# Kernel tuning notes

Hardware: AMD Instinct MI355X
Metric: run time of the kernel (lower is better)

## Reference

```python
import jax, jax.numpy as jnp
import numpy as np

EPS = 1e-5
N, K, C = 32768, 27, 128


def setup_inputs() -> dict:
    key = jax.random.key(0)
    k1, k2, k3, k4 = jax.random.split(key, 4)
    feats = jax.random.normal(k1, (N, C), dtype=jnp.float32)
    # Precomputed kernel-offset neighbor map (MinkowskiEngine kernel map),
    # one input index per (point, kernel offset).
    neighbors = jax.random.randint(k2, (N, K), 0, N, dtype=jnp.int32)
    scale = 1.0 / np.sqrt(K * C)  # fan-in init like sparse conv
    W1 = jax.random.normal(k3, (K, C, C), dtype=jnp.float32) * scale
    W2 = jax.random.normal(k4, (K, C, C), dtype=jnp.float32) * scale
    g1 = jnp.ones((C,), jnp.float32)
    b1 = jnp.zeros((C,), jnp.float32)
    g2 = jnp.ones((C,), jnp.float32)
    b2 = jnp.zeros((C,), jnp.float32)
    return {"feats": feats, "neighbors": neighbors, "W1": W1, "g1": g1,
            "b1": b1, "W2": W2, "g2": g2, "b2": b2}


def _sparse_conv(f, nbr, W):
    # gather-GEMM-scatter: gather neighbor features per kernel offset,
    # contract with that offset's weight, sum over offsets.
    gathered = f[nbr]                      # [N, K, C]
    return jnp.einsum('nkc,kcd->nd', gathered, W)  # [N, C]


def _batch_norm(x, gamma, beta):
    mu = jnp.mean(x, axis=0)
    var = jnp.mean(jnp.square(x - mu), axis=0)
    return (x - mu) * jax.lax.rsqrt(var + EPS) * gamma + beta


def reference(feats, neighbors, W1, g1, b1, W2, g2, b2):
    out = _sparse_conv(feats, neighbors, W1)
    out = jax.nn.relu(_batch_norm(out, g1, b1))
    out = _sparse_conv(out, neighbors, W2)
    out = _batch_norm(out, g2, b2)
    return jax.nn.relu(out + feats)
```

## Files before the change

### kernel.cpp

```cpp
#include <hip/hip_runtime.h>
#include <stdint.h>

#define NPTS 32768
#define KOFF 27
#define CH   128
#define NC   (NPTS*CH)
#define TILE_M 64
#define NITER (KOFF*2)

typedef __attribute__((ext_vector_type(8))) short short8;
typedef __attribute__((ext_vector_type(4))) float f32x4;
typedef unsigned short u16;

__device__ __forceinline__ float bf2f(u16 u) {
    union { uint32_t i; float f; } v; v.i = ((uint32_t)u) << 16; return v.f;
}
__device__ __forceinline__ u16 f2bf(float f) {
    union { float f; uint32_t i; } v; v.f = f;
    return (u16)((v.i + 0x7FFF + ((v.i >> 16) & 1)) >> 16);
}

#define GLDS16(gp, lp) __builtin_amdgcn_global_load_lds( \
    (__attribute__((address_space(1))) void*)(gp),           \
    (__attribute__((address_space(3))) void*)(lp), 16, 0, 0)

__global__ __launch_bounds__(256)
void prep_kernel(const float* __restrict__ W1, const float* __restrict__ W2,
                 u16* __restrict__ W1t, u16* __restrict__ W2t,
                 const float* __restrict__ feats, u16* __restrict__ xbuf,
                 float* __restrict__ stat)
{
    __shared__ u16 t[128*129];
    const int b = blockIdx.x, tid = threadIdx.x;
    if (b < 2*KOFF) {
        if (b == 0) for (int i = tid; i < 512; i += 256) stat[i] = 0.0f;
        const float* src = (b < KOFF) ? W1 + (size_t)b*CH*CH : W2 + (size_t)(b-KOFF)*CH*CH;
        u16* dst         = (b < KOFF) ? W1t + (size_t)b*CH*CH : W2t + (size_t)(b-KOFF)*CH*CH;
        for (int e = tid; e < CH*CH; e += 256) {
            int c = e >> 7, d = e & 127;
            t[d*129 + c] = f2bf(src[e]);
        }
        __syncthreads();
        for (int e = tid; e < CH*CH; e += 256) {
            int d = e >> 7, c = e & 127;
            dst[e] = t[d*129 + c];
        }
    } else {
        size_t e = ((size_t)(b - 2*KOFF) * 256 + tid) * 8;
        float4 a = *(const float4*)(feats + e);
        float4 c = *(const float4*)(feats + e + 4);
        ushort4 lo, hi;
        lo.x = f2bf(a.x); lo.y = f2bf(a.y); lo.z = f2bf(a.z); lo.w = f2bf(a.w);
        hi.x = f2bf(c.x); hi.y = f2bf(c.y); hi.z = f2bf(c.z); hi.w = f2bf(c.w);
        *(ushort4*)(xbuf + e) = lo;
        *(ushort4*)(xbuf + e + 4) = hi;
    }
}

__global__ __launch_bounds__(256)
void ResidualBlock_77498389889548_kernel(const u16* __restrict__ xb,
                                         const int* __restrict__ nbr,
                                         const u16* __restrict__ Wt,
                                         u16* __restrict__ y,
                                         float* __restrict__ gsum,
                                         float* __restrict__ gsq)
{
    __shared__ __align__(16) u16 A_lds[2][TILE_M*64];
    __shared__ __align__(16) u16 B_lds[2][CH*64];
    __shared__ int idx_lds[KOFF*TILE_M];
    __shared__ float ls[CH], lq[CH];

    const int tid = threadIdx.x;
    const int n0  = blockIdx.x * TILE_M;

    if (tid < CH) { ls[tid] = 0.0f; lq[tid] = 0.0f; }
    for (int e = tid; e < KOFF*TILE_M; e += 256) {
        int kk = e >> 6, r = e & 63;
        int nb = nbr[(size_t)(n0 + r)*KOFF + kk];
        idx_lds[e] = ((unsigned)nb < (unsigned)NPTS) ? nb : 0;
    }
    __syncthreads();

    const int wave = tid >> 6;
    const int lane = tid & 63;
    const int wrow = (wave >> 1) * 32;
    const int wcol = (wave & 1) * 64;
    const int lm   = lane & 15;
    const int quad = lane >> 4;
    const int l8r  = lane >> 3;
    const int swz  = ((lane & 7) ^ l8r) << 3;

    f32x4 acc[2][4];
    #pragma unroll
    for (int i = 0; i < 2; ++i)
        #pragma unroll
        for (int j = 0; j < 4; ++j)
            #pragma unroll
            for (int r = 0; r < 4; ++r) acc[i][j][r] = 0.0f;

    int aoff[2][2], boff[2][4];
    #pragma unroll
    for (int kc = 0; kc < 2; ++kc) {
        int g = kc*4 + quad;
        #pragma unroll
        for (int i = 0; i < 2; ++i) {
            int row = wrow + i*16 + lm;
            aoff[kc][i] = row*128 + ((g ^ (row & 7)) << 4);
        }
        #pragma unroll
        for (int j = 0; j < 4; ++j) {
            int d = wcol + j*16 + lm;
            boff[kc][j] = d*128 + ((g ^ (d & 7)) << 4);
        }
    }

    auto stage = [&](int it, int b) {
        const int kk = it >> 1;
        const int h  = it & 1;
        #pragma unroll
        for (int j = 0; j < 2; ++j) {
            int row8 = wave*16 + j*8;
            int nb = idx_lds[kk*64 + row8 + l8r];
            GLDS16(xb + (size_t)nb*CH + h*64 + swz, &A_lds[b][row8*64]);
        }
        const u16* wb = Wt + (size_t)kk*CH*CH + h*64 + swz;
        #pragma unroll
        for (int j = 0; j < 4; ++j) {
            int row8 = wave*32 + j*8;
            GLDS16(wb + (size_t)(row8 + l8r)*CH, &B_lds[b][row8*64]);
        }
    };

    stage(0, 0);
    __syncthreads();

    for (int it = 0; it < NITER; ++it) {
        const int cur = it & 1;
        if (it + 1 < NITER) stage(it + 1, cur ^ 1);

        const char* Ab = (const char*)A_lds[cur];
        const char* Bb = (const char*)B_lds[cur];
        #pragma unroll
        for (int kc = 0; kc < 2; ++kc) {
            short8 a[2], b[4];
            #pragma unroll
            for (int i = 0; i < 2; ++i) a[i] = *(const short8*)(Ab + aoff[kc][i]);
            #pragma unroll
            for (int j = 0; j < 4; ++j) b[j] = *(const short8*)(Bb + boff[kc][j]);
            #pragma unroll
            for (int i = 0; i < 2; ++i)
                #pragma unroll
                for (int j = 0; j < 4; ++j)
                    acc[i][j] = __builtin_amdgcn_mfma_f32_16x16x32_bf16(a[i], b[j], acc[i][j], 0, 0, 0);
        }
        __syncthreads();
    }

    const int colb = wcol + lm;
    #pragma unroll
    for (int i = 0; i < 2; ++i) {
        #pragma unroll
        for (int r = 0; r < 4; ++r) {
            int row = n0 + wrow + i*16 + quad*4 + r;
            u16* yp = y + (size_t)row*CH + colb;
            #pragma unroll
            for (int j = 0; j < 4; ++j) yp[j*16] = f2bf(acc[i][j][r]);
        }
    }
    #pragma unroll
    for (int j = 0; j < 4; ++j) {
        float s = 0.0f, q = 0.0f;
        #pragma unroll
        for (int i = 0; i < 2; ++i)
            #pragma unroll
            for (int r = 0; r < 4; ++r) {
                float v = acc[i][j][r];
                s += v; q += v*v;
            }
        atomicAdd(&ls[colb + j*16], s);
        atomicAdd(&lq[colb + j*16], q);
    }
    __syncthreads();
    if (tid < CH) {
        atomicAdd(&gsum[tid], ls[tid]);
        atomicAdd(&gsq[tid],  lq[tid]);
    }
}

__global__ __launch_bounds__(256)
void norm_relu_kernel(const u16* __restrict__ y, const float* __restrict__ sums,
                      const float* __restrict__ sumsq, const float* __restrict__ gam,
                      const float* __restrict__ bet, u16* __restrict__ xo)
{
    __shared__ float sc[128], sh[128];
    const int tid = threadIdx.x;
    if (tid < 128) {
        float mu  = sums[tid] * (1.0f/NPTS);
        float var = fmaxf(sumsq[tid] * (1.0f/NPTS) - mu*mu, 0.0f);
        float rs  = rsqrtf(var + 1e-5f);
        float s   = rs * gam[tid];
        sc[tid] = s; sh[tid] = bet[tid] - mu*s;
    }
    __syncthreads();
    size_t e = ((size_t)blockIdx.x*256 + tid) * 8;
    int c0 = (int)(e & 127);
    ushort4 lo = *(const ushort4*)(y + e);
    ushort4 hi = *(const ushort4*)(y + e + 4);
    ushort4 o0, o1;
    o0.x = f2bf(fmaxf(bf2f(lo.x)*sc[c0+0] + sh[c0+0], 0.0f));
    o0.y = f2bf(fmaxf(bf2f(lo.y)*sc[c0+1] + sh[c0+1], 0.0f));
    o0.z = f2bf(fmaxf(bf2f(lo.z)*sc[c0+2] + sh[c0+2], 0.0f));
    o0.w = f2bf(fmaxf(bf2f(lo.w)*sc[c0+3] + sh[c0+3], 0.0f));
    o1.x = f2bf(fmaxf(bf2f(hi.x)*sc[c0+4] + sh[c0+4], 0.0f));
    o1.y = f2bf(fmaxf(bf2f(hi.y)*sc[c0+5] + sh[c0+5], 0.0f));
    o1.z = f2bf(fmaxf(bf2f(hi.z)*sc[c0+6] + sh[c0+6], 0.0f));
    o1.w = f2bf(fmaxf(bf2f(hi.w)*sc[c0+7] + sh[c0+7], 0.0f));
    *(ushort4*)(xo + e) = o0;
    *(ushort4*)(xo + e + 4) = o1;
}

__global__ __launch_bounds__(256)
void final_kernel(const u16* __restrict__ y, const float* __restrict__ sums,
                  const float* __restrict__ sumsq, const float* __restrict__ gam,
                  const float* __restrict__ bet, const float* __restrict__ feats,
                  float* __restrict__ out)
{
    __shared__ float sc[128], sh[128];
    const int tid = threadIdx.x;
    if (tid < 128) {
        float mu  = sums[tid] * (1.0f/NPTS);
        float var = fmaxf(sumsq[tid] * (1.0f/NPTS) - mu*mu, 0.0f);
        float rs  = rsqrtf(var + 1e-5f);
        float s   = rs * gam[tid];
        sc[tid] = s; sh[tid] = bet[tid] - mu*s;
    }
    __syncthreads();
    size_t e = ((size_t)blockIdx.x*256 + tid) * 4;
    int c0 = (int)(e & 127);
    ushort4 in = *(const ushort4*)(y + e);
    float4 ft = *(const float4*)(feats + e);
    float4 o;
    o.x = fmaxf(bf2f(in.x)*sc[c0+0] + sh[c0+0] + ft.x, 0.0f);
    o.y = fmaxf(bf2f(in.y)*sc[c0+1] + sh[c0+1] + ft.y, 0.0f);
    o.z = fmaxf(bf2f(in.z)*sc[c0+2] + sh[c0+2] + ft.z, 0.0f);
    o.w = fmaxf(bf2f(in.w)*sc[c0+3] + sh[c0+3] + ft.w, 0.0f);
    *(float4*)(out + e) = o;
}

extern "C" void kernel_launch(void* const* d_in, const int* in_sizes, int n_in,
                              void* d_out, int out_size, void* d_ws, size_t ws_size,
                              hipStream_t stream)
{
    const float* feats = (const float*)d_in[0];
    const int*   nbr   = (const int*)d_in[1];
    const float* W1    = (const float*)d_in[2];
    const float* g1    = (const float*)d_in[3];
    const float* b1    = (const float*)d_in[4];
    const float* W2    = (const float*)d_in[5];
    const float* g2    = (const float*)d_in[6];
    const float* b2    = (const float*)d_in[7];
    float* out = (float*)d_out;

    char* ws = (char*)d_ws;
    u16*   xbuf = (u16*)ws;
    u16*   ybuf = xbuf + (size_t)NC;
    u16*   W1t  = ybuf + (size_t)NC;
    u16*   W2t  = W1t + (size_t)KOFF*CH*CH;
    float* stat = (float*)(W2t + (size_t)KOFF*CH*CH);

    prep_kernel<<<dim3(2*KOFF + NC/2048), 256, 0, stream>>>(W1, W2, W1t, W2t, feats, xbuf, stat);

    ResidualBlock_77498389889548_kernel<<<dim3(NPTS/TILE_M), 256, 0, stream>>>(
        xbuf, nbr, W1t, ybuf, stat, stat + 128);
    norm_relu_kernel<<<dim3(NC/2048), 256, 0, stream>>>(ybuf, stat, stat + 128, g1, b1, xbuf);

    ResidualBlock_77498389889548_kernel<<<dim3(NPTS/TILE_M), 256, 0, stream>>>(
        xbuf, nbr, W2t, ybuf, stat + 256, stat + 384);
    final_kernel<<<dim3(NC/1024), 256, 0, stream>>>(ybuf, stat + 256, stat + 384, g2, b2, feats, out);
}
```

Baseline: 232.5 us.

## Halve sparse-conv tile rows and drop LDS double buffering

Reduces the gather-GEMM tile from 64 to 32 points per block and replaces the double-buffered LDS staging with a single buffer that is loaded, synchronised, then consumed each iteration. This lowers LDS and register use per block and doubles the grid, aiming for higher occupancy to hide gather latency. In exchange, each block re-reads the full weight slice for half as many rows, so weight traffic doubles, and load/compute overlap inside a block is lost.

```diff
diff --git a/kernel.cpp b/kernel.cpp
--- a/kernel.cpp
+++ b/kernel.cpp
@@ -5,7 +5,7 @@
 #define KOFF 27
 #define CH   128
 #define NC   (NPTS*CH)
-#define TILE_M 64
+#define TILE_M 32
 #define NITER (KOFF*2)
 
 typedef __attribute__((ext_vector_type(8))) short short8;
@@ -65,8 +65,8 @@
                                          float* __restrict__ gsum,
                                          float* __restrict__ gsq)
 {
-    __shared__ __align__(16) u16 A_lds[2][TILE_M*64];
-    __shared__ __align__(16) u16 B_lds[2][CH*64];
+    __shared__ __align__(16) u16 A_lds[TILE_M*64];
+    __shared__ __align__(16) u16 B_lds[CH*64];
     __shared__ int idx_lds[KOFF*TILE_M];
     __shared__ float ls[CH], lq[CH];
 
@@ -75,7 +75,7 @@
 
     if (tid < CH) { ls[tid] = 0.0f; lq[tid] = 0.0f; }
     for (int e = tid; e < KOFF*TILE_M; e += 256) {
-        int kk = e >> 6, r = e & 63;
+        int kk = e >> 5, r = e & 31;
         int nb = nbr[(size_t)(n0 + r)*KOFF + kk];
         idx_lds[e] = ((unsigned)nb < (unsigned)NPTS) ? nb : 0;
     }
@@ -83,30 +83,25 @@
 
     const int wave = tid >> 6;
     const int lane = tid & 63;
-    const int wrow = (wave >> 1) * 32;
+    const int wrow = (wave >> 1) * 16;
     const int wcol = (wave & 1) * 64;
     const int lm   = lane & 15;
     const int quad = lane >> 4;
     const int l8r  = lane >> 3;
     const int swz  = ((lane & 7) ^ l8r) << 3;
 
-    f32x4 acc[2][4];
-    #pragma unroll
-    for (int i = 0; i < 2; ++i)
-        #pragma unroll
-        for (int j = 0; j < 4; ++j)
-            #pragma unroll
-            for (int r = 0; r < 4; ++r) acc[i][j][r] = 0.0f;
-
-    int aoff[2][2], boff[2][4];
+    f32x4 acc[4];
+    #pragma unroll
+    for (int j = 0; j < 4; ++j)
+        #pragma unroll
+        for (int r = 0; r < 4; ++r) acc[j][r] = 0.0f;
+
+    int aoff[2], boff[2][4];
     #pragma unroll
     for (int kc = 0; kc < 2; ++kc) {
         int g = kc*4 + quad;
-        #pragma unroll
-        for (int i = 0; i < 2; ++i) {
-            int row = wrow + i*16 + lm;
-            aoff[kc][i] = row*128 + ((g ^ (row & 7)) << 4);
-        }
+        int row = wrow + lm;
+        aoff[kc] = row*128 + ((g ^ (row & 7)) << 4);
         #pragma unroll
         for (int j = 0; j < 4; ++j) {
             int d = wcol + j*16 + lm;
@@ -114,71 +109,56 @@
         }
     }
 
-    auto stage = [&](int it, int b) {
+    const char* Ab = (const char*)A_lds;
+    const char* Bb = (const char*)B_lds;
+
+    for (int it = 0; it < NITER; ++it) {
         const int kk = it >> 1;
         const int h  = it & 1;
-        #pragma unroll
-        for (int j = 0; j < 2; ++j) {
-            int row8 = wave*16 + j*8;
-            int nb = idx_lds[kk*64 + row8 + l8r];
-            GLDS16(xb + (size_t)nb*CH + h*64 + swz, &A_lds[b][row8*64]);
+
+        {
+            int row8 = wave*8;
+            int nb = idx_lds[kk*32 + row8 + l8r];
+            GLDS16(xb + (size_t)nb*CH + h*64 + swz, &A_lds[row8*64]);
         }
         const u16* wb = Wt + (size_t)kk*CH*CH + h*64 + swz;
         #pragma unroll
         for (int j = 0; j < 4; ++j) {
             int row8 = wave*32 + j*8;
-            GLDS16(wb + (size_t)(row8 + l8r)*CH, &B_lds[b][row8*64]);
-        }
-    };
-
-    stage(0, 0);
-    __syncthreads();
-
-    for (int it = 0; it < NITER; ++it) {
-        const int cur = it & 1;
-        if (it + 1 < NITER) stage(it + 1, cur ^ 1);
-
-        const char* Ab = (const char*)A_lds[cur];
-        const char* Bb = (const char*)B_lds[cur];
+            GLDS16(wb + (size_t)(row8 + l8r)*CH, &B_lds[row8*64]);
+        }
+        __syncthreads();
+
         #pragma unroll
         for (int kc = 0; kc < 2; ++kc) {
-            short8 a[2], b[4];
-            #pragma unroll
-            for (int i = 0; i < 2; ++i) a[i] = *(const short8*)(Ab + aoff[kc][i]);
+            short8 a = *(const short8*)(Ab + aoff[kc]);
+            short8 b[4];
             #pragma unroll
             for (int j = 0; j < 4; ++j) b[j] = *(const short8*)(Bb + boff[kc][j]);
             #pragma unroll
-            for (int i = 0; i < 2; ++i)
-                #pragma unroll
-                for (int j = 0; j < 4; ++j)
-                    acc[i][j] = __builtin_amdgcn_mfma_f32_16x16x32_bf16(a[i], b[j], acc[i][j], 0, 0, 0);
+            for (int j = 0; j < 4; ++j)
+                acc[j] = __builtin_amdgcn_mfma_f32_16x16x32_bf16(a, b[j], acc[j], 0, 0, 0);
         }
         __syncthreads();
     }
 
-    const int colb = wcol + lm;
-    #pragma unroll
-    for (int i = 0; i < 2; ++i) {
-        #pragma unroll
-        for (int r = 0; r < 4; ++r) {
-            int row = n0 + wrow + i*16 + quad*4 + r;
-            u16* yp = y + (size_t)row*CH + colb;
-            #pragma unroll
-            for (int j = 0; j < 4; ++j) yp[j*16] = f2bf(acc[i][j][r]);
-        }
+    #pragma unroll
+    for (int r = 0; r < 4; ++r) {
+        int row = n0 + wrow + quad*4 + r;
+        u16* yp = y + (size_t)row*CH + wcol + lm;
+        #pragma unroll
+        for (int j = 0; j < 4; ++j) yp[j*16] = f2bf(acc[j][r]);
     }
     #pragma unroll
     for (int j = 0; j < 4; ++j) {
         float s = 0.0f, q = 0.0f;
         #pragma unroll
-        for (int i = 0; i < 2; ++i)
-            #pragma unroll
-            for (int r = 0; r < 4; ++r) {
-                float v = acc[i][j][r];
-                s += v; q += v*v;
-            }
-        atomicAdd(&ls[colb + j*16], s);
-        atomicAdd(&lq[colb + j*16], q);
+        for (int r = 0; r < 4; ++r) {
+            float v = acc[j][r];
+            s += v; q += v*v;
+        }
+        atomicAdd(&ls[wcol + j*16 + lm], s);
+        atomicAdd(&lq[wcol + j*16 + lm], q);
     }
     __syncthreads();
     if (tid < CH) {
```

After: 250.8 us. +7.8%, slower.

## Split kernel offsets across three blocks and reduce partials in a separate stats kernel

Applied to the files above, without the earlier changes.

The gather-GEMM kernel now splits the 27 kernel offsets into 3 groups over a second grid dimension. Each block writes its bf16 partial sum to its own buffer, and a new sumstats kernel adds the three partials, writes y and accumulates the batch-norm statistics. The GEMM loop drops LDS double buffering and adds launch_bounds(256,5) to raise occupancy. The aim is more parallelism and better latency hiding in exchange for extra memory traffic for the partials, two extra kernel launches, no load/compute overlap within a block, and extra bf16 rounding of the partials.

```diff
diff --git a/kernel.cpp b/kernel.cpp
--- a/kernel.cpp
+++ b/kernel.cpp
@@ -5,8 +5,10 @@
 #define KOFF 27
 #define CH   128
 #define NC   (NPTS*CH)
+#define KSPLIT 3
+#define KPG  9
 #define TILE_M 64
-#define NITER (KOFF*2)
+#define NITER (KPG*2)
 
 typedef __attribute__((ext_vector_type(8))) short short8;
 typedef __attribute__((ext_vector_type(4))) float f32x4;
@@ -57,26 +59,23 @@
     }
 }
 
-__global__ __launch_bounds__(256)
+__global__ __launch_bounds__(256, 5)
 void ResidualBlock_77498389889548_kernel(const u16* __restrict__ xb,
                                          const int* __restrict__ nbr,
                                          const u16* __restrict__ Wt,
-                                         u16* __restrict__ y,
-                                         float* __restrict__ gsum,
-                                         float* __restrict__ gsq)
-{
-    __shared__ __align__(16) u16 A_lds[2][TILE_M*64];
-    __shared__ __align__(16) u16 B_lds[2][CH*64];
-    __shared__ int idx_lds[KOFF*TILE_M];
-    __shared__ float ls[CH], lq[CH];
+                                         u16* __restrict__ part)
+{
+    __shared__ __align__(16) u16 A_lds[TILE_M*64];
+    __shared__ __align__(16) u16 B_lds[CH*64];
+    __shared__ int idx_lds[KPG*TILE_M];
 
     const int tid = threadIdx.x;
     const int n0  = blockIdx.x * TILE_M;
-
-    if (tid < CH) { ls[tid] = 0.0f; lq[tid] = 0.0f; }
-    for (int e = tid; e < KOFF*TILE_M; e += 256) {
+    const int kg  = blockIdx.y;
+
+    for (int e = tid; e < KPG*TILE_M; e += 256) {
         int kk = e >> 6, r = e & 63;
-        int nb = nbr[(size_t)(n0 + r)*KOFF + kk];
+        int nb = nbr[(size_t)(n0 + r)*KOFF + kg*KPG + kk];
         idx_lds[e] = ((unsigned)nb < (unsigned)NPTS) ? nb : 0;
     }
     __syncthreads();
@@ -114,32 +113,27 @@
         }
     }
 
-    auto stage = [&](int it, int b) {
+    const char* Ab = (const char*)A_lds;
+    const char* Bb = (const char*)B_lds;
+
+    for (int it = 0; it < NITER; ++it) {
         const int kk = it >> 1;
         const int h  = it & 1;
+
         #pragma unroll
         for (int j = 0; j < 2; ++j) {
             int row8 = wave*16 + j*8;
             int nb = idx_lds[kk*64 + row8 + l8r];
-            GLDS16(xb + (size_t)nb*CH + h*64 + swz, &A_lds[b][row8*64]);
-        }
-        const u16* wb = Wt + (size_t)kk*CH*CH + h*64 + swz;
+            GLDS16(xb + (size_t)nb*CH + h*64 + swz, &A_lds[row8*64]);
+        }
+        const u16* wb = Wt + (size_t)(kg*KPG + kk)*CH*CH + h*64 + swz;
         #pragma unroll
         for (int j = 0; j < 4; ++j) {
             int row8 = wave*32 + j*8;
-            GLDS16(wb + (size_t)(row8 + l8r)*CH, &B_lds[b][row8*64]);
-        }
-    };
-
-    stage(0, 0);
-    __syncthreads();
-
-    for (int it = 0; it < NITER; ++it) {
-        const int cur = it & 1;
-        if (it + 1 < NITER) stage(it + 1, cur ^ 1);
-
-        const char* Ab = (const char*)A_lds[cur];
-        const char* Bb = (const char*)B_lds[cur];
+            GLDS16(wb + (size_t)(row8 + l8r)*CH, &B_lds[row8*64]);
+        }
+        __syncthreads();
+
         #pragma unroll
         for (int kc = 0; kc < 2; ++kc) {
             short8 a[2], b[4];
@@ -156,29 +150,63 @@
         __syncthreads();
     }
 
+    u16* pb = part + (size_t)kg * NC;
     const int colb = wcol + lm;
     #pragma unroll
     for (int i = 0; i < 2; ++i) {
         #pragma unroll
         for (int r = 0; r < 4; ++r) {
             int row = n0 + wrow + i*16 + quad*4 + r;
-            u16* yp = y + (size_t)row*CH + colb;
-            #pragma unroll
-            for (int j = 0; j < 4; ++j) yp[j*16] = f2bf(acc[i][j][r]);
-        }
-    }
-    #pragma unroll
-    for (int j = 0; j < 4; ++j) {
-        float s = 0.0f, q = 0.0f;
-        #pragma unroll
-        for (int i = 0; i < 2; ++i)
-            #pragma unroll
-            for (int r = 0; r < 4; ++r) {
-                float v = acc[i][j][r];
-                s += v; q += v*v;
-            }
-        atomicAdd(&ls[colb + j*16], s);
-        atomicAdd(&lq[colb + j*16], q);
+            u16* pp = pb + (size_t)row*CH + colb;
+            #pragma unroll
+            for (int j = 0; j < 4; ++j) pp[j*16] = f2bf(acc[i][j][r]);
+        }
+    }
+}
+
+__global__ __launch_bounds__(256)
+void sumstats_kernel(const u16* __restrict__ p0, const u16* __restrict__ p1,
+                     const u16* __restrict__ p2, u16* __restrict__ y,
+                     float* __restrict__ gsum, float* __restrict__ gsq)
+{
+    __shared__ float ls[CH], lq[CH];
+    const int tid = threadIdx.x;
+    const int c8 = (tid & 15) * 8;
+    const int r0 = tid >> 4;
+    const int b = blockIdx.x;
+    if (tid < CH) { ls[tid] = 0.0f; lq[tid] = 0.0f; }
+    __syncthreads();
+
+    float s[8], q[8];
+    #pragma unroll
+    for (int i = 0; i < 8; ++i) { s[i] = 0.0f; q[i] = 0.0f; }
+
+    for (int r = r0; r < 128; r += 16) {
+        size_t e = (size_t)(b*128 + r)*CH + c8;
+        ushort4 a0 = *(const ushort4*)(p0 + e), a1 = *(const ushort4*)(p0 + e + 4);
+        ushort4 b0 = *(const ushort4*)(p1 + e), b1 = *(const ushort4*)(p1 + e + 4);
+        ushort4 d0 = *(const ushort4*)(p2 + e), d1 = *(const ushort4*)(p2 + e + 4);
+        float v[8];
+        v[0] = bf2f(a0.x) + bf2f(b0.x) + bf2f(d0.x);
+        v[1] = bf2f(a0.y) + bf2f(b0.y) + bf2f(d0.y);
+        v[2] = bf2f(a0.z) + bf2f(b0.z) + bf2f(d0.z);
+        v[3] = bf2f(a0.w) + bf2f(b0.w) + bf2f(d0.w);
+        v[4] = bf2f(a1.x) + bf2f(b1.x) + bf2f(d1.x);
+        v[5] = bf2f(a1.y) + bf2f(b1.y) + bf2f(d1.y);
+        v[6] = bf2f(a1.z) + bf2f(b1.z) + bf2f(d1.z);
+        v[7] = bf2f(a1.w) + bf2f(b1.w) + bf2f(d1.w);
+        ushort4 o0, o1;
+        o0.x = f2bf(v[0]); o0.y = f2bf(v[1]); o0.z = f2bf(v[2]); o0.w = f2bf(v[3]);
+        o1.x = f2bf(v[4]); o1.y = f2bf(v[5]); o1.z = f2bf(v[6]); o1.w = f2bf(v[7]);
+        *(ushort4*)(y + e) = o0;
+        *(ushort4*)(y + e + 4) = o1;
+        #pragma unroll
+        for (int i = 0; i < 8; ++i) { s[i] += v[i]; q[i] += v[i]*v[i]; }
+    }
+    #pragma unroll
+    for (int i = 0; i < 8; ++i) {
+        atomicAdd(&ls[c8 + i], s[i]);
+        atomicAdd(&lq[c8 + i], q[i]);
     }
     __syncthreads();
     if (tid < CH) {
@@ -263,18 +291,23 @@
 
     char* ws = (char*)d_ws;
     u16*   xbuf = (u16*)ws;
-    u16*   ybuf = xbuf + (size_t)NC;
+    u16*   prt  = xbuf + (size_t)NC;
+    u16*   ybuf = prt + (size_t)3*NC;
     u16*   W1t  = ybuf + (size_t)NC;
     u16*   W2t  = W1t + (size_t)KOFF*CH*CH;
     float* stat = (float*)(W2t + (size_t)KOFF*CH*CH);
 
     prep_kernel<<<dim3(2*KOFF + NC/2048), 256, 0, stream>>>(W1, W2, W1t, W2t, feats, xbuf, stat);
 
-    ResidualBlock_77498389889548_kernel<<<dim3(NPTS/TILE_M), 256, 0, stream>>>(
-        xbuf, nbr, W1t, ybuf, stat, stat + 128);
+    ResidualBlock_77498389889548_kernel<<<dim3(NPTS/TILE_M, KSPLIT), 256, 0, stream>>>(
+        xbuf, nbr, W1t, prt);
+    sumstats_kernel<<<dim3(NPTS/128), 256, 0, stream>>>(
+        prt, prt + (size_t)NC, prt + (size_t)2*NC, ybuf, stat, stat + 128);
     norm_relu_kernel<<<dim3(NC/2048), 256, 0, stream>>>(ybuf, stat, stat + 128, g1, b1, xbuf);
 
-    ResidualBlock_77498389889548_kernel<<<dim3(NPTS/TILE_M), 256, 0, stream>>>(
-        xbuf, nbr, W2t, ybuf, stat + 256, stat + 384);
+    ResidualBlock_77498389889548_kernel<<<dim3(NPTS/TILE_M, KSPLIT), 256, 0, stream>>>(
+        xbuf, nbr, W2t, prt);
+    sumstats_kernel<<<dim3(NPTS/128), 256, 0, stream>>>(
+        prt, prt + (size_t)NC, prt + (size_t)2*NC, ybuf, stat + 256, stat + 384);
     final_kernel<<<dim3(NC/1024), 256, 0, stream>>>(ybuf, stat + 256, stat + 384, g2, b2, feats, out);
 }
```

After: 222.5 us. 4.3% less time.
